# Kernel tuning notes

Measured on AMD Instinct MI355X. Metric: run time of the kernel, lower is better.

Reference implementation:

```python
import jax, jax.numpy as jnp
import numpy as np

NUM_HEADS = 8


def setup_inputs() -> dict:
    key = jax.random.key(0)
    ks = jax.random.split(key, 7)
    B, Tq, Tkv, J, C = 16, 243, 243, 17, 256
    q = jax.random.normal(ks[0], (B, Tq, J, C), dtype=jnp.float32)
    kv = jax.random.normal(ks[1], (B, Tkv, J, C), dtype=jnp.float32)
    s = 1.0 / np.sqrt(C)
    Wq = jax.random.normal(ks[2], (C, C), dtype=jnp.float32) * s
    Wk = jax.random.normal(ks[3], (C, C), dtype=jnp.float32) * s
    Wv = jax.random.normal(ks[4], (C, C), dtype=jnp.float32) * s
    Wp = jax.random.normal(ks[5], (C, C), dtype=jnp.float32) * s
    bp = jnp.zeros((C,), dtype=jnp.float32)
    return {"q": q, "kv": kv, "Wq": Wq, "Wk": Wk, "Wv": Wv, "Wp": Wp, "bp": bp}


def reference(q, kv, Wq, Wk, Wv, Wp, bp):
    # q: [B, Tq, J, C], kv: [B, Tkv, J, C]
    b, tq, j, d = q.shape
    t_kv = kv.shape[1]
    h = NUM_HEADS
    hd = d // h
    scale = hd ** (-0.5)

    def split_heads(x, t):
        # [B, T, J, C] -> [B, H, J, T, hd]  (matches permute(0,3,2,1,4))
        return x.reshape(b, t, j, h, hd).transpose(0, 3, 2, 1, 4)

    q_p = split_heads(q @ Wq.T, tq)
    k_p = split_heads(kv @ Wk.T, t_kv)
    v_p = split_heads(kv @ Wv.T, t_kv)

    # attn: [B, H, J, Tq, Tkv]
    attn = jnp.einsum('bhjqe,bhjke->bhjqk', q_p, k_p) * scale
    attn = jax.nn.softmax(attn, axis=-1)
    # out: [B, H, J, Tq, hd] -> [B, Tq, J, C]
    out = jnp.einsum('bhjqk,bhjke->bhjqe', attn, v_p)
    out = out.transpose(0, 3, 2, 1, 4).reshape(b, tq, j, d)
    out = out @ Wp.T + bp
    return (attn, out)
```

## Files before the change

### kernel.cpp

```cpp
#include <hip/hip_runtime.h>

typedef _Float16 f16;
typedef _Float16 f16x8 __attribute__((ext_vector_type(8)));
typedef float f32x4 __attribute__((ext_vector_type(4)));

#define B_DIM 16
#define T_DIM 243
#define J_DIM 17
#define C_DIM 256
#define H_DIM 8
#define HD_DIM 32
#define M_DIM (B_DIM * T_DIM * J_DIM)
#define NSLICE (B_DIM * H_DIM * J_DIM)
#define TJ (T_DIM * J_DIM)

#define QP_OFF 0ull
#define KP_OFF ((unsigned long long)NSLICE * T_DIM * HD_DIM)
#define VPT_OFF (2ull * KP_OFF)
#define O_OFF (VPT_OFF + (unsigned long long)NSLICE * HD_DIM * 256)
#define WF_OFF (O_OFF + (unsigned long long)M_DIM * C_DIM)
#define ATTN_SZ ((unsigned long long)NSLICE * T_DIM * T_DIM)

#define SWZ(row, col) ((col) ^ (((row) & 7) << 3))

__global__ __launch_bounds__(256)
void wconv_kernel(const float* __restrict__ Wq, const float* __restrict__ Wk,
                  const float* __restrict__ Wv, const float* __restrict__ Wp,
                  f16* __restrict__ wf)
{
    int i = blockIdx.x * 256 + threadIdx.x;
    const float* src = (i < 65536) ? Wq : (i < 131072) ? Wk : (i < 196608) ? Wv : Wp;
    wf[i] = (f16)src[i & 65535];
}

__global__ __launch_bounds__(256)
void proj_kernel(const float* __restrict__ q, const float* __restrict__ kv,
                 const f16* __restrict__ wf, f16* __restrict__ ws)
{
    const int which = blockIdx.z;
    const float* A = (which == 0) ? q : kv;
    const f16* W = wf + which * 65536;
    f16* out = ws + (which == 0 ? QP_OFF : KP_OFF);

    const int tid = threadIdx.x;
    const int w = tid >> 6, l = tid & 63;
    const int lm = l & 15, g = l >> 4;
    const int m0 = blockIdx.x * 64;
    const int n0 = blockIdx.y * 64;

    int arow = m0 + w * 16 + lm;
    if (arow > M_DIM - 1) arow = M_DIM - 1;
    const float* Ab = A + (size_t)arow * C_DIM + g * 8;

    f16x8 af[8];
#pragma unroll
    for (int kk = 0; kk < 8; ++kk) {
        f32x4 a0 = *(const f32x4*)(Ab + kk * 32);
        f32x4 a1 = *(const f32x4*)(Ab + kk * 32 + 4);
#pragma unroll
        for (int j = 0; j < 4; ++j) { af[kk][j] = (f16)a0[j]; af[kk][4 + j] = (f16)a1[j]; }
    }

    f32x4 acc[4] = {};
#pragma unroll
    for (int nt = 0; nt < 4; ++nt) {
        const f16* Wb = W + (size_t)(n0 + nt * 16 + lm) * C_DIM + g * 8;
#pragma unroll
        for (int kk = 0; kk < 8; ++kk) {
            f16x8 bf = *(const f16x8*)(Wb + kk * 32);
            acc[nt] = __builtin_amdgcn_mfma_f32_16x16x32_f16(af[kk], bf, acc[nt], 0, 0, 0);
        }
    }

#pragma unroll
    for (int nt = 0; nt < 4; ++nt) {
        int n = n0 + nt * 16 + lm;
        int h = n >> 5, e = n & 31;
#pragma unroll
        for (int r = 0; r < 4; ++r) {
            int m = m0 + w * 16 + g * 4 + r;
            if (m >= M_DIM) continue;
            int b = m / TJ;
            int rem = m - b * TJ;
            int t = rem / J_DIM;
            int jj = rem - t * J_DIM;
            int s = (b * H_DIM + h) * J_DIM + jj;
            size_t idx = (size_t)s * (T_DIM * HD_DIM) + (size_t)t * HD_DIM + e;
            out[idx] = (f16)acc[nt][r];
        }
    }
}

__global__ __launch_bounds__(256)
void vproj_kernel(const float* __restrict__ kv, const f16* __restrict__ wv,
                  f16* __restrict__ vpt)
{
    __shared__ f16 Sv[64 * 72];

    const int bj = blockIdx.z;
    const int b = bj / J_DIM, j = bj - b * J_DIM;
    const int t0 = blockIdx.x * 64;
    const int n0 = blockIdx.y * 64;

    const int tid = threadIdx.x;
    const int w = tid >> 6, l = tid & 63;
    const int lm = l & 15, g = l >> 4;

    int t = t0 + w * 16 + lm;
    if (t > T_DIM - 1) t = T_DIM - 1;
    const float* Ab = kv + ((size_t)b * TJ + (size_t)t * J_DIM + j) * C_DIM + g * 8;

    f16x8 af[8];
#pragma unroll
    for (int kk = 0; kk < 8; ++kk) {
        f32x4 a0 = *(const f32x4*)(Ab + kk * 32);
        f32x4 a1 = *(const f32x4*)(Ab + kk * 32 + 4);
#pragma unroll
        for (int jj = 0; jj < 4; ++jj) { af[kk][jj] = (f16)a0[jj]; af[kk][4 + jj] = (f16)a1[jj]; }
    }

    f32x4 acc[4] = {};
#pragma unroll
    for (int nt = 0; nt < 4; ++nt) {
        const f16* Wb = wv + (size_t)(n0 + nt * 16 + lm) * C_DIM + g * 8;
#pragma unroll
        for (int kk = 0; kk < 8; ++kk) {
            f16x8 bf = *(const f16x8*)(Wb + kk * 32);
            acc[nt] = __builtin_amdgcn_mfma_f32_16x16x32_f16(af[kk], bf, acc[nt], 0, 0, 0);
        }
    }

    const int trow = w * 16 + g * 4;
#pragma unroll
    for (int nt = 0; nt < 4; ++nt) {
        int nl = nt * 16 + lm;
#pragma unroll
        for (int r = 0; r < 4; ++r)
            Sv[nl * 72 + trow + r] = (f16)acc[nt][r];
    }
    __syncthreads();

    const int nl = tid >> 2, tp = tid & 3;
    const int n = n0 + nl;
    const int h = n >> 5, e = n & 31;
    const int s = (b * H_DIM + h) * J_DIM + j;
    const int tbase = t0 + tp * 16;

    f16x8 v0 = *(const f16x8*)&Sv[nl * 72 + tp * 16];
    f16x8 v1 = *(const f16x8*)&Sv[nl * 72 + tp * 16 + 8];
    if (tbase + 15 > T_DIM - 1) {
#pragma unroll
        for (int i = 0; i < 8; ++i) {
            if (tbase + i > T_DIM - 1) v0[i] = (f16)0;
            if (tbase + 8 + i > T_DIM - 1) v1[i] = (f16)0;
        }
    }
    f16* dst = vpt + (size_t)s * (HD_DIM * 256) + (size_t)e * 256 + tbase;
    *(f16x8*)dst = v0;
    *(f16x8*)(dst + 8) = v1;
}

__global__ __launch_bounds__(256)
void attn_kernel(const f16* __restrict__ ws_qp, const f16* __restrict__ ws_kp,
                 const f16* __restrict__ ws_vpt, f16* __restrict__ ws_o,
                 float* __restrict__ attn_out)
{
    __shared__ f16 S[64 * 256];

    const int s = blockIdx.y;
    const int q0 = blockIdx.x * 64;
    const int tid = threadIdx.x;
    const int w = tid >> 6, l = tid & 63;
    const int lm = l & 15, g = l >> 4;
    const float scale = 0.17677669529663687f;

    const f16* qpS = ws_qp + (size_t)s * (T_DIM * HD_DIM);
    const f16* kpS = ws_kp + (size_t)s * (T_DIM * HD_DIM);

    int qrow = q0 + w * 16 + lm;
    if (qrow > T_DIM - 1) qrow = T_DIM - 1;
    f16x8 aq = *(const f16x8*)(qpS + qrow * HD_DIM + g * 8);

    float cv[16][4];
    f32x4 zero = {0.f, 0.f, 0.f, 0.f};
#pragma unroll
    for (int kt = 0; kt < 16; ++kt) {
        int krow = kt * 16 + lm;
        if (krow > T_DIM - 1) krow = T_DIM - 1;
        f16x8 bk = *(const f16x8*)(kpS + krow * HD_DIM + g * 8);
        f32x4 c = __builtin_amdgcn_mfma_f32_16x16x32_f16(aq, bk, zero, 0, 0, 0);
#pragma unroll
        for (int r = 0; r < 4; ++r) cv[kt][r] = c[r] * scale;
    }
    if (lm >= 3) {
#pragma unroll
        for (int r = 0; r < 4; ++r) cv[15][r] = -1e30f;
    }

    float mx[4], sm[4], rinv[4];
#pragma unroll
    for (int r = 0; r < 4; ++r) {
        float m = cv[0][r];
#pragma unroll
        for (int kt = 1; kt < 16; ++kt) m = fmaxf(m, cv[kt][r]);
        m = fmaxf(m, __shfl_xor(m, 1));
        m = fmaxf(m, __shfl_xor(m, 2));
        m = fmaxf(m, __shfl_xor(m, 4));
        m = fmaxf(m, __shfl_xor(m, 8));
        mx[r] = m;
        float t = 0.f;
#pragma unroll
        for (int kt = 0; kt < 16; ++kt) {
            float p = __expf(cv[kt][r] - m);
            cv[kt][r] = p;
            t += p;
        }
        t += __shfl_xor(t, 1);
        t += __shfl_xor(t, 2);
        t += __shfl_xor(t, 4);
        t += __shfl_xor(t, 8);
        sm[r] = t;
        rinv[r] = 1.0f / t;
    }

    float* dst = attn_out + (size_t)s * (T_DIM * T_DIM);
    const int rowb = w * 16 + g * 4;
#pragma unroll
    for (int r = 0; r < 4; ++r) {
        const int qr = q0 + rowb + r;
        const bool rok = qr < T_DIM;
        float* drow = dst + (size_t)qr * T_DIM;
#pragma unroll
        for (int kt = 0; kt < 16; ++kt) {
            float p = cv[kt][r] * rinv[r];
            int col = kt * 16 + lm;
            S[(rowb + r) * 256 + SWZ(rowb + r, col)] = (f16)p;
            if (rok && col < T_DIM) drow[col] = p;
        }
    }
    __syncthreads();

    const f16* vpS = ws_vpt + (size_t)s * (HD_DIM * 256);
    f32x4 o0 = {}, o1 = {};
    const int prow = w * 16 + lm;
#pragma unroll
    for (int kk = 0; kk < 8; ++kk) {
        f16x8 ap = *(const f16x8*)(&S[prow * 256 + SWZ(prow, kk * 32 + g * 8)]);
        f16x8 b0 = *(const f16x8*)(vpS + (size_t)(0 * 16 + lm) * 256 + kk * 32 + g * 8);
        f16x8 b1 = *(const f16x8*)(vpS + (size_t)(1 * 16 + lm) * 256 + kk * 32 + g * 8);
        o0 = __builtin_amdgcn_mfma_f32_16x16x32_f16(ap, b0, o0, 0, 0, 0);
        o1 = __builtin_amdgcn_mfma_f32_16x16x32_f16(ap, b1, o1, 0, 0, 0);
    }

    int b = s / (H_DIM * J_DIM);
    int rem = s - b * (H_DIM * J_DIM);
    int h = rem / J_DIM;
    int jj = rem - h * J_DIM;
#pragma unroll
    for (int r = 0; r < 4; ++r) {
        int qr = q0 + w * 16 + g * 4 + r;
        if (qr >= T_DIM) continue;
        size_t m = (size_t)b * TJ + (size_t)qr * J_DIM + jj;
        ws_o[m * 256 + h * 32 + lm] = (f16)o0[r];
        ws_o[m * 256 + h * 32 + 16 + lm] = (f16)o1[r];
    }
}

__global__ __launch_bounds__(256)
void outproj_kernel(const f16* __restrict__ ws_o, const f16* __restrict__ wpf,
                    const float* __restrict__ bp, float* __restrict__ out)
{
    const int tid = threadIdx.x;
    const int w = tid >> 6, l = tid & 63;
    const int lm = l & 15, g = l >> 4;
    const int m0 = blockIdx.x * 64;
    const int n0 = blockIdx.y * 64;

    int arow = m0 + w * 16 + lm;
    if (arow > M_DIM - 1) arow = M_DIM - 1;
    const f16* Ab = ws_o + (size_t)arow * C_DIM + g * 8;
    f16x8 af[8];
#pragma unroll
    for (int kk = 0; kk < 8; ++kk) af[kk] = *(const f16x8*)(Ab + kk * 32);

    f32x4 acc[4] = {};
#pragma unroll
    for (int nt = 0; nt < 4; ++nt) {
        const f16* Wb = wpf + (size_t)(n0 + nt * 16 + lm) * C_DIM + g * 8;
#pragma unroll
        for (int kk = 0; kk < 8; ++kk) {
            f16x8 bf = *(const f16x8*)(Wb + kk * 32);
            acc[nt] = __builtin_amdgcn_mfma_f32_16x16x32_f16(af[kk], bf, acc[nt], 0, 0, 0);
        }
    }

#pragma unroll
    for (int nt = 0; nt < 4; ++nt) {
        int n = n0 + nt * 16 + lm;
        float bias = bp[n];
#pragma unroll
        for (int r = 0; r < 4; ++r) {
            int m = m0 + w * 16 + g * 4 + r;
            if (m < M_DIM) out[(size_t)m * C_DIM + n] = acc[nt][r] + bias;
        }
    }
}

extern "C" void kernel_launch(void* const* d_in, const int* in_sizes, int n_in,
                              void* d_out, int out_size, void* d_ws, size_t ws_size,
                              hipStream_t stream)
{
    const float* q  = (const float*)d_in[0];
    const float* kv = (const float*)d_in[1];
    const float* Wq = (const float*)d_in[2];
    const float* Wk = (const float*)d_in[3];
    const float* Wv = (const float*)d_in[4];
    const float* Wp = (const float*)d_in[5];
    const float* bp = (const float*)d_in[6];
    float* attn_out = (float*)d_out;
    float* out = attn_out + ATTN_SZ;
    f16* ws = (f16*)d_ws;

    wconv_kernel<<<dim3(1024), dim3(256), 0, stream>>>(Wq, Wk, Wv, Wp, ws + WF_OFF);

    dim3 gp((M_DIM + 63) / 64, 4, 2);
    proj_kernel<<<gp, dim3(256), 0, stream>>>(q, kv, ws + WF_OFF, ws);

    dim3 gv(4, 4, B_DIM * J_DIM);
    vproj_kernel<<<gv, dim3(256), 0, stream>>>(kv, ws + WF_OFF + 2 * 65536, ws + VPT_OFF);

    dim3 ga(4, NSLICE);
    attn_kernel<<<ga, dim3(256), 0, stream>>>(ws + QP_OFF, ws + KP_OFF, ws + VPT_OFF,
                                              ws + O_OFF, attn_out);

    dim3 go((M_DIM + 63) / 64, 4);
    outproj_kernel<<<go, dim3(256), 0, stream>>>(ws + O_OFF, ws + WF_OFF + 3 * 65536, bp, out);
}
```

Baseline: 601.7 us.

## Swap MFMA operands for row-contiguous outputs and vectorize stores; cover full N per block

The projection and output-projection kernels swap the MFMA A/B operands so each lane holds four consecutive output columns of one row. That allows vectorized f16x4 and float4 stores. Each block now computes all 256 output columns, so the fp32 activations are read and converted once instead of four times, at the cost of 64 accumulator registers per thread. The attention kernel also transposes QK^T so each lane owns one query row. Its softmax reductions shrink to two cross-group shuffles, and the attention probabilities are written as float4 stores instead of scalar strided stores.

```diff
diff --git a/kernel.cpp b/kernel.cpp
--- a/kernel.cpp
+++ b/kernel.cpp
@@ -2,7 +2,9 @@
 
 typedef _Float16 f16;
 typedef _Float16 f16x8 __attribute__((ext_vector_type(8)));
+typedef _Float16 f16x4 __attribute__((ext_vector_type(4)));
 typedef float f32x4 __attribute__((ext_vector_type(4)));
+typedef float f32x4a __attribute__((ext_vector_type(4), aligned(4)));
 
 #define B_DIM 16
 #define T_DIM 243
@@ -46,10 +48,10 @@
     const int w = tid >> 6, l = tid & 63;
     const int lm = l & 15, g = l >> 4;
     const int m0 = blockIdx.x * 64;
-    const int n0 = blockIdx.y * 64;
 
     int arow = m0 + w * 16 + lm;
-    if (arow > M_DIM - 1) arow = M_DIM - 1;
+    const bool mok = arow < M_DIM;
+    if (!mok) arow = M_DIM - 1;
     const float* Ab = A + (size_t)arow * C_DIM + g * 8;
 
     f16x8 af[8];
@@ -61,32 +63,31 @@
         for (int j = 0; j < 4; ++j) { af[kk][j] = (f16)a0[j]; af[kk][4 + j] = (f16)a1[j]; }
     }
 
-    f32x4 acc[4] = {};
-#pragma unroll
-    for (int nt = 0; nt < 4; ++nt) {
-        const f16* Wb = W + (size_t)(n0 + nt * 16 + lm) * C_DIM + g * 8;
+    f32x4 acc[16] = {};
+#pragma unroll
+    for (int nt = 0; nt < 16; ++nt) {
+        const f16* Wb = W + (size_t)(nt * 16 + lm) * C_DIM + g * 8;
 #pragma unroll
         for (int kk = 0; kk < 8; ++kk) {
             f16x8 bf = *(const f16x8*)(Wb + kk * 32);
-            acc[nt] = __builtin_amdgcn_mfma_f32_16x16x32_f16(af[kk], bf, acc[nt], 0, 0, 0);
-        }
-    }
-
-#pragma unroll
-    for (int nt = 0; nt < 4; ++nt) {
-        int n = n0 + nt * 16 + lm;
-        int h = n >> 5, e = n & 31;
-#pragma unroll
-        for (int r = 0; r < 4; ++r) {
-            int m = m0 + w * 16 + g * 4 + r;
-            if (m >= M_DIM) continue;
-            int b = m / TJ;
-            int rem = m - b * TJ;
-            int t = rem / J_DIM;
-            int jj = rem - t * J_DIM;
-            int s = (b * H_DIM + h) * J_DIM + jj;
-            size_t idx = (size_t)s * (T_DIM * HD_DIM) + (size_t)t * HD_DIM + e;
-            out[idx] = (f16)acc[nt][r];
+            acc[nt] = __builtin_amdgcn_mfma_f32_16x16x32_f16(bf, af[kk], acc[nt], 0, 0, 0);
+        }
+    }
+
+    int b = arow / TJ;
+    int rem = arow - b * TJ;
+    int t = rem / J_DIM;
+    int jj = rem - t * J_DIM;
+    if (mok) {
+#pragma unroll
+        for (int nt = 0; nt < 16; ++nt) {
+            int n0 = nt * 16 + g * 4;
+            int h = n0 >> 5, e = n0 & 31;
+            int sI = (b * H_DIM + h) * J_DIM + jj;
+            f16x4 v;
+#pragma unroll
+            for (int r = 0; r < 4; ++r) v[r] = (f16)acc[nt][r];
+            *(f16x4*)(out + (size_t)sI * (T_DIM * HD_DIM) + (size_t)t * HD_DIM + e) = v;
         }
     }
 }
@@ -178,8 +179,9 @@
     const f16* kpS = ws_kp + (size_t)s * (T_DIM * HD_DIM);
 
     int qrow = q0 + w * 16 + lm;
-    if (qrow > T_DIM - 1) qrow = T_DIM - 1;
-    f16x8 aq = *(const f16x8*)(qpS + qrow * HD_DIM + g * 8);
+    const bool qok = qrow < T_DIM;
+    if (!qok) qrow = T_DIM - 1;
+    f16x8 bq = *(const f16x8*)(qpS + qrow * HD_DIM + g * 8);
 
     float cv[16][4];
     f32x4 zero = {0.f, 0.f, 0.f, 0.f};
@@ -187,55 +189,62 @@
     for (int kt = 0; kt < 16; ++kt) {
         int krow = kt * 16 + lm;
         if (krow > T_DIM - 1) krow = T_DIM - 1;
-        f16x8 bk = *(const f16x8*)(kpS + krow * HD_DIM + g * 8);
-        f32x4 c = __builtin_amdgcn_mfma_f32_16x16x32_f16(aq, bk, zero, 0, 0, 0);
+        f16x8 ak = *(const f16x8*)(kpS + krow * HD_DIM + g * 8);
+        f32x4 c = __builtin_amdgcn_mfma_f32_16x16x32_f16(ak, bq, zero, 0, 0, 0);
 #pragma unroll
         for (int r = 0; r < 4; ++r) cv[kt][r] = c[r] * scale;
     }
-    if (lm >= 3) {
-#pragma unroll
-        for (int r = 0; r < 4; ++r) cv[15][r] = -1e30f;
-    }
-
-    float mx[4], sm[4], rinv[4];
-#pragma unroll
-    for (int r = 0; r < 4; ++r) {
-        float m = cv[0][r];
-#pragma unroll
-        for (int kt = 1; kt < 16; ++kt) m = fmaxf(m, cv[kt][r]);
-        m = fmaxf(m, __shfl_xor(m, 1));
-        m = fmaxf(m, __shfl_xor(m, 2));
-        m = fmaxf(m, __shfl_xor(m, 4));
-        m = fmaxf(m, __shfl_xor(m, 8));
-        mx[r] = m;
-        float t = 0.f;
-#pragma unroll
-        for (int kt = 0; kt < 16; ++kt) {
-            float p = __expf(cv[kt][r] - m);
-            cv[kt][r] = p;
-            t += p;
-        }
-        t += __shfl_xor(t, 1);
-        t += __shfl_xor(t, 2);
-        t += __shfl_xor(t, 4);
-        t += __shfl_xor(t, 8);
-        sm[r] = t;
-        rinv[r] = 1.0f / t;
-    }
-
-    float* dst = attn_out + (size_t)s * (T_DIM * T_DIM);
-    const int rowb = w * 16 + g * 4;
-#pragma unroll
-    for (int r = 0; r < 4; ++r) {
-        const int qr = q0 + rowb + r;
-        const bool rok = qr < T_DIM;
-        float* drow = dst + (size_t)qr * T_DIM;
-#pragma unroll
-        for (int kt = 0; kt < 16; ++kt) {
-            float p = cv[kt][r] * rinv[r];
-            int col = kt * 16 + lm;
-            S[(rowb + r) * 256 + SWZ(rowb + r, col)] = (f16)p;
-            if (rok && col < T_DIM) drow[col] = p;
+#pragma unroll
+    for (int r = 0; r < 4; ++r)
+        if (g * 4 + r >= 3) cv[15][r] = -1e30f;
+
+    float mx = -1e30f;
+#pragma unroll
+    for (int kt = 0; kt < 16; ++kt) {
+        float a = fmaxf(fmaxf(cv[kt][0], cv[kt][1]), fmaxf(cv[kt][2], cv[kt][3]));
+        mx = fmaxf(mx, a);
+    }
+    mx = fmaxf(mx, __shfl_xor(mx, 16));
+    mx = fmaxf(mx, __shfl_xor(mx, 32));
+
+    float s0 = 0.f, s1 = 0.f;
+#pragma unroll
+    for (int kt = 0; kt < 16; ++kt) {
+        float p0 = __expf(cv[kt][0] - mx);
+        float p1 = __expf(cv[kt][1] - mx);
+        float p2 = __expf(cv[kt][2] - mx);
+        float p3 = __expf(cv[kt][3] - mx);
+        cv[kt][0] = p0; cv[kt][1] = p1; cv[kt][2] = p2; cv[kt][3] = p3;
+        s0 += p0 + p1;
+        s1 += p2 + p3;
+    }
+    float sum = s0 + s1;
+    sum += __shfl_xor(sum, 16);
+    sum += __shfl_xor(sum, 32);
+    const float rinv = 1.0f / sum;
+
+    float* drow = attn_out + (size_t)s * (T_DIM * T_DIM) + (size_t)qrow * T_DIM;
+    const int qlocal = w * 16 + lm;
+#pragma unroll
+    for (int kt = 0; kt < 16; ++kt) {
+        const int col0 = kt * 16 + g * 4;
+        f16x4 pv4;
+        f32x4a o4;
+#pragma unroll
+        for (int r = 0; r < 4; ++r) {
+            float p = cv[kt][r] * rinv;
+            o4[r] = p;
+            pv4[r] = (f16)p;
+        }
+        *(f16x4*)&S[qlocal * 256 + SWZ(qlocal, col0)] = pv4;
+        if (qok) {
+            if (col0 + 3 < T_DIM) {
+                *(f32x4a*)(drow + col0) = o4;
+            } else if (col0 < T_DIM) {
+                drow[col0] = o4[0];
+                drow[col0 + 1] = o4[1];
+                drow[col0 + 2] = o4[2];
+            }
         }
     }
     __syncthreads();
@@ -274,34 +283,35 @@
     const int w = tid >> 6, l = tid & 63;
     const int lm = l & 15, g = l >> 4;
     const int m0 = blockIdx.x * 64;
-    const int n0 = blockIdx.y * 64;
-
-    int arow = m0 + w * 16 + lm;
-    if (arow > M_DIM - 1) arow = M_DIM - 1;
-    const f16* Ab = ws_o + (size_t)arow * C_DIM + g * 8;
+
+    int m = m0 + w * 16 + lm;
+    const bool mok = m < M_DIM;
+    if (!mok) m = M_DIM - 1;
+    const f16* Ab = ws_o + (size_t)m * C_DIM + g * 8;
     f16x8 af[8];
 #pragma unroll
     for (int kk = 0; kk < 8; ++kk) af[kk] = *(const f16x8*)(Ab + kk * 32);
 
-    f32x4 acc[4] = {};
-#pragma unroll
-    for (int nt = 0; nt < 4; ++nt) {
-        const f16* Wb = wpf + (size_t)(n0 + nt * 16 + lm) * C_DIM + g * 8;
+    f32x4 acc[16] = {};
+#pragma unroll
+    for (int nt = 0; nt < 16; ++nt) {
+        const f16* Wb = wpf + (size_t)(nt * 16 + lm) * C_DIM + g * 8;
 #pragma unroll
         for (int kk = 0; kk < 8; ++kk) {
             f16x8 bf = *(const f16x8*)(Wb + kk * 32);
-            acc[nt] = __builtin_amdgcn_mfma_f32_16x16x32_f16(af[kk], bf, acc[nt], 0, 0, 0);
-        }
-    }
-
-#pragma unroll
-    for (int nt = 0; nt < 4; ++nt) {
-        int n = n0 + nt * 16 + lm;
-        float bias = bp[n];
-#pragma unroll
-        for (int r = 0; r < 4; ++r) {
-            int m = m0 + w * 16 + g * 4 + r;
-            if (m < M_DIM) out[(size_t)m * C_DIM + n] = acc[nt][r] + bias;
+            acc[nt] = __builtin_amdgcn_mfma_f32_16x16x32_f16(bf, af[kk], acc[nt], 0, 0, 0);
+        }
+    }
+
+    if (mok) {
+#pragma unroll
+        for (int nt = 0; nt < 16; ++nt) {
+            int n0 = nt * 16 + g * 4;
+            f32x4a bv = *(const f32x4a*)(bp + n0);
+            f32x4a o;
+#pragma unroll
+            for (int r = 0; r < 4; ++r) o[r] = acc[nt][r] + bv[r];
+            *(f32x4a*)(out + (size_t)m * C_DIM + n0) = o;
         }
     }
 }
@@ -323,7 +333,7 @@
 
     wconv_kernel<<<dim3(1024), dim3(256), 0, stream>>>(Wq, Wk, Wv, Wp, ws + WF_OFF);
 
-    dim3 gp((M_DIM + 63) / 64, 4, 2);
+    dim3 gp((M_DIM + 63) / 64, 1, 2);
     proj_kernel<<<gp, dim3(256), 0, stream>>>(q, kv, ws + WF_OFF, ws);
 
     dim3 gv(4, 4, B_DIM * J_DIM);
@@ -333,6 +343,6 @@
     attn_kernel<<<ga, dim3(256), 0, stream>>>(ws + QP_OFF, ws + KP_OFF, ws + VPT_OFF,
                                               ws + O_OFF, attn_out);
 
-    dim3 go((M_DIM + 63) / 64, 4);
+    dim3 go((M_DIM + 63) / 64, 1);
     outproj_kernel<<<go, dim3(256), 0, stream>>>(ws + O_OFF, ws + WF_OFF + 3 * 65536, bp, out);
 }
```

Measured after the change: 598.7 us. About the same (-0.5%).
